# Optimization experiments

Hardware: AMD Instinct MI355X
Metric: run time of the kernel (lower is better)

Reference implementation:

```python
import jax, jax.numpy as jnp
import numpy as np

N_CELL = 50000
N_GENE = 50000
E = 800000
D = 256
EPS = 1e-5


def setup_inputs() -> dict:
    key = jax.random.key(0)
    ks = jax.random.split(key, 12)
    inp = {
        "x_cell": jax.random.normal(ks[0], (N_CELL, D), jnp.float32),
        "x_gene": jax.random.normal(ks[1], (N_GENE, D), jnp.float32),
        "W_cg": jax.random.normal(ks[2], (D, D), jnp.float32) * (1.0 / np.sqrt(D)),
        "W_gc": jax.random.normal(ks[3], (D, D), jnp.float32) * (1.0 / np.sqrt(D)),
        "W_gg": jax.random.normal(ks[4], (D, D), jnp.float32) * (1.0 / np.sqrt(D)),
        "gamma_cell": jnp.ones((D,), jnp.float32),
        "beta_cell": jnp.zeros((D,), jnp.float32),
        "gamma_gene": jnp.ones((D,), jnp.float32),
        "beta_gene": jnp.zeros((D,), jnp.float32),
        "b_cell": jnp.zeros((D,), jnp.float32),
        "b_gene": jnp.zeros((D,), jnp.float32),
        "src_cg": jax.random.randint(ks[5], (E,), 0, N_CELL, jnp.int64 if jax.config.jax_enable_x64 else jnp.int32),
        "dst_cg": jax.random.randint(ks[6], (E,), 0, N_GENE, jnp.int64 if jax.config.jax_enable_x64 else jnp.int32),
        "src_gc": jax.random.randint(ks[7], (E,), 0, N_GENE, jnp.int64 if jax.config.jax_enable_x64 else jnp.int32),
        "dst_gc": jax.random.randint(ks[8], (E,), 0, N_CELL, jnp.int64 if jax.config.jax_enable_x64 else jnp.int32),
        "src_gg": jax.random.randint(ks[9], (E,), 0, N_GENE, jnp.int64 if jax.config.jax_enable_x64 else jnp.int32),
        "dst_gg": jax.random.randint(ks[10], (E,), 0, N_GENE, jnp.int64 if jax.config.jax_enable_x64 else jnp.int32),
    }
    return inp


def _graph_conv(x_src, src, dst, n_src, n_dst, W):
    """DGL GraphConv with norm='both': D_dst^{-1/2} A D_src^{-1/2} X W."""
    ones = jnp.ones(src.shape[0], x_src.dtype)
    deg_out = jnp.clip(jax.ops.segment_sum(ones, src, num_segments=n_src), 1.0)
    deg_in = jnp.clip(jax.ops.segment_sum(ones, dst, num_segments=n_dst), 1.0)
    h = x_src * jax.lax.rsqrt(deg_out)[:, None]          # [n_src, D]
    agg = jax.ops.segment_sum(h[src], dst, num_segments=n_dst)  # gather+scatter
    agg = agg * jax.lax.rsqrt(deg_in)[:, None]           # [n_dst, D]
    return agg @ W


def _post(h, gamma, beta, b):
    # LayerNorm (affine) -> + h_bias -> relu -> dropout(p=0, eval = identity)
    mu = jnp.mean(h, axis=-1, keepdims=True)
    var = jnp.mean((h - mu) ** 2, axis=-1, keepdims=True)
    h = (h - mu) * jax.lax.rsqrt(var + EPS) * gamma + beta
    return jax.nn.relu(h + b)


def reference(x_cell, x_gene, W_cg, W_gc, W_gg, gamma_cell, beta_cell,
              gamma_gene, beta_gene, b_cell, b_gene,
              src_cg, dst_cg, src_gc, dst_gc, src_gg, dst_gg):
    # HeteroGraphConv with aggregate='sum' across relations per dst ntype
    h_gene = (_graph_conv(x_cell, src_cg, dst_cg, N_CELL, N_GENE, W_cg)
              + _graph_conv(x_gene, src_gg, dst_gg, N_GENE, N_GENE, W_gg))
    h_cell = _graph_conv(x_gene, src_gc, dst_gc, N_GENE, N_CELL, W_gc)
    out_cell = _post(h_cell, gamma_cell, beta_cell, b_cell)
    out_gene = _post(h_gene, gamma_gene, beta_gene, b_gene)
    return jnp.stack([out_cell, out_gene])  # [2, 50000, 256]
```

## Files before the change

### kernel.cpp

```cpp
#include <hip/hip_runtime.h>
#include <hip/hip_bf16.h>
#include <stdint.h>

#define DDIM 256
#define NSHARD 8
#define T1 4096
#define NCPAD 128
#define CCAP 9216

typedef short s8v __attribute__((ext_vector_type(8)));
typedef float f4v __attribute__((ext_vector_type(4)));

__device__ __forceinline__ float bf2f(unsigned u) { return __uint_as_float(u << 16); }
__device__ __forceinline__ unsigned short f2bf(float f) {
    __hip_bfloat16 h = __float2bfloat16(f);
    return *reinterpret_cast<unsigned short*>(&h);
}
__device__ __forceinline__ unsigned pack2(float a, float b) {
    return (unsigned)f2bf(a) | ((unsigned)f2bf(b) << 16);
}

__global__ void transpose3_k(const float* __restrict__ W0, const float* __restrict__ W1,
                             const float* __restrict__ W2, __hip_bfloat16* __restrict__ T0,
                             __hip_bfloat16* __restrict__ T1v, __hip_bfloat16* __restrict__ T2) {
    const float* W = (blockIdx.y == 0) ? W0 : (blockIdx.y == 1) ? W1 : W2;
    __hip_bfloat16* T = (blockIdx.y == 0) ? T0 : (blockIdx.y == 1) ? T1v : T2;
    T[blockIdx.x * DDIM + threadIdx.x] = __float2bfloat16(W[threadIdx.x * DDIM + blockIdx.x]);
}

__global__ __launch_bounds__(256) void bin1_k(
    const int* __restrict__ s0, const int* __restrict__ d0,
    const int* __restrict__ s1, const int* __restrict__ d1,
    const int* __restrict__ s2, const int* __restrict__ d2,
    int* __restrict__ cs_shard,
    int* __restrict__ gcur,
    unsigned* __restrict__ recs,
    int N, int E) {
    __shared__ unsigned stage[T1];
    __shared__ int hcnt[NCPAD], hoff[NCPAD], lbase[NCPAD], lcur[NCPAD];
    const int t = threadIdx.x;
    const int rel = blockIdx.y;
    const int* s = (rel == 0) ? s0 : (rel == 1) ? s1 : s2;
    const int* d = (rel == 0) ? d0 : (rel == 1) ? d1 : d2;
    const int e0 = blockIdx.x * T1;
    const int n = min(T1, E - e0);
    int* csb = cs_shard + ((size_t)(blockIdx.x & (NSHARD - 1)) * 3 + rel) * N;

    if (t < NCPAD) { hcnt[t] = 0; lcur[t] = 0; }
    __syncthreads();

    int ssr[T1 / 256], ddr[T1 / 256];
    #pragma unroll
    for (int k = 0; k < T1 / 256; ++k) {
        const int li = k * 256 + t;
        const bool v = li < n;
        ssr[k] = v ? s[e0 + li] : -1;
        ddr[k] = v ? d[e0 + li] : -1;
        if (v) {
            atomicAdd(&hcnt[ddr[k] >> 9], 1);
            atomicAdd(&csb[ssr[k]], 1);
        }
    }
    __syncthreads();

    if (t < 64) {
        const int a0 = hcnt[2 * t], a1 = hcnt[2 * t + 1];
        const int sum = a0 + a1;
        int incl = sum;
        #pragma unroll
        for (int off = 1; off < 64; off <<= 1) {
            const int u = __shfl_up(incl, off);
            if (t >= off) incl += u;
        }
        const int excl = incl - sum;
        hoff[2 * t] = excl;
        hoff[2 * t + 1] = excl + a0;
    }
    __syncthreads();
    if (t < NCPAD) lbase[t] = atomicAdd(&gcur[rel * NCPAD + t], hcnt[t]);
    __syncthreads();

    #pragma unroll
    for (int k = 0; k < T1 / 256; ++k) {
        if (ddr[k] >= 0) {
            const int b = ddr[k] >> 9;
            const int p = atomicAdd(&lcur[b], 1);
            stage[hoff[b] + p] = (unsigned)ssr[k] | ((unsigned)(ddr[k] & 511) << 16)
                                 | ((unsigned)b << 25);
        }
    }
    __syncthreads();

    for (int i = t; i < n; i += 256) {
        const unsigned r = stage[i];
        const int b = (int)(r >> 25);
        const int pos = lbase[b] + (i - hoff[b]);
        if (pos < CCAP)
            recs[((size_t)rel * NCPAD + b) * CCAP + pos] = r & 0x1FFFFFFu;
    }
}

__global__ void reduce_cs_k(const int* __restrict__ cs_shard, int* __restrict__ cs, int n3) {
    const int i = blockIdx.x * blockDim.x + threadIdx.x;
    if (i >= n3) return;
    int v = 0;
    #pragma unroll
    for (int s = 0; s < NSHARD; ++s) v += cs_shard[(size_t)s * n3 + i];
    cs[i] = v;
}

__global__ __launch_bounds__(256) void sort_k(
    unsigned* __restrict__ recs, const int* __restrict__ gcur,
    int* __restrict__ row_beg, int* __restrict__ row_cnt, int N, int ncb) {
    __shared__ unsigned stage[CCAP];
    __shared__ int rc[512], ro[512], rcur[512];
    const int t = threadIdx.x;
    const int rel = blockIdx.x / ncb, bin = blockIdx.x % ncb;
    const size_t base = ((size_t)rel * NCPAD + bin) * CCAP;
    const int n = min(gcur[rel * NCPAD + bin], CCAP);

    for (int i = t; i < 512; i += 256) rc[i] = 0;
    __syncthreads();
    for (int i = t; i < n; i += 256) {
        const unsigned r = recs[base + i];
        stage[i] = r;
        atomicAdd(&rc[(r >> 16) & 511], 1);
    }
    __syncthreads();
    if (t < 64) {
        int v[8], p[8], sum = 0;
        #pragma unroll
        for (int j = 0; j < 8; ++j) { v[j] = rc[t * 8 + j]; p[j] = sum; sum += v[j]; }
        int incl = sum;
        #pragma unroll
        for (int off = 1; off < 64; off <<= 1) {
            const int u = __shfl_up(incl, off);
            if (t >= off) incl += u;
        }
        const int excl = incl - sum;
        #pragma unroll
        for (int j = 0; j < 8; ++j) { ro[t * 8 + j] = excl + p[j]; rcur[t * 8 + j] = excl + p[j]; }
    }
    __syncthreads();
    for (int i = t; i < 512; i += 256) {
        const int grow = bin * 512 + i;
        if (grow < N) {
            row_cnt[(size_t)rel * N + grow] = rc[i];
            row_beg[(size_t)rel * N + grow] = (int)(base + ro[i]);
        }
    }
    for (int i = t; i < n; i += 256) {
        const unsigned r = stage[i];
        const int pos = atomicAdd(&rcur[(r >> 16) & 511], 1);
        recs[base + pos] = r & 0xffffu;
    }
}

__global__ __launch_bounds__(256, 4) void gemm2_k(
    const float* __restrict__ X,
    const __hip_bfloat16* __restrict__ Wt0, const __hip_bfloat16* __restrict__ Wt1,
    const int* __restrict__ deg0, const int* __restrict__ deg1,
    __hip_bfloat16* __restrict__ Y0, __hip_bfloat16* __restrict__ Y1, int M) {
    __shared__ __hip_bfloat16 wlds[2][2][16][DDIM];
    const int t = threadIdx.x;
    const int lane = t & 63, wid = t >> 6;
    const int c = lane & 15, kb = lane >> 4;
    const int rA = blockIdx.x * 128 + wid * 32 + c;
    const int rB = rA + 16;
    const bool vA = rA < M, vB = rB < M;
    const int rAc = vA ? rA : (M - 1), rBc = vB ? rB : (M - 1);

    s8v xfA[8], xfB[8];
    const float* xA = X + (size_t)rAc * DDIM;
    const float* xB = X + (size_t)rBc * DDIM;
    #pragma unroll
    for (int ks = 0; ks < 8; ++ks) {
        const int k0 = ks * 32 + kb * 8;
        const f4v a0 = *reinterpret_cast<const f4v*>(xA + k0);
        const f4v a1 = *reinterpret_cast<const f4v*>(xA + k0 + 4);
        const f4v b0 = *reinterpret_cast<const f4v*>(xB + k0);
        const f4v b1 = *reinterpret_cast<const f4v*>(xB + k0 + 4);
        union { s8v v; unsigned short u[8]; } fa, fb;
        #pragma unroll
        for (int j = 0; j < 4; ++j) {
            fa.u[j] = f2bf(a0[j]); fa.u[4 + j] = f2bf(a1[j]);
            fb.u[j] = f2bf(b0[j]); fb.u[4 + j] = f2bf(b1[j]);
        }
        xfA[ks] = fa.v; xfB[ks] = fb.v;
    }

    const int dA0 = deg0[rAc], dB0 = deg0[rBc], dA1 = deg1[rAc], dB1 = deg1[rBc];
    const float s0A = rsqrtf((float)(dA0 < 1 ? 1 : dA0));
    const float s0B = rsqrtf((float)(dB0 < 1 ? 1 : dB0));
    const float s1A = rsqrtf((float)(dA1 < 1 ? 1 : dA1));
    const float s1B = rsqrtf((float)(dB1 < 1 ? 1 : dB1));

    {
        #pragma unroll
        for (int j = 0; j < 4; ++j) {
            const int q = t + j * 256;
            const int rel = q >> 9, rt = (q >> 5) & 15, ch = q & 31;
            const __hip_bfloat16* Wsrc = rel ? Wt1 : Wt0;
            const uint4 v = *reinterpret_cast<const uint4*>(Wsrc + (size_t)rt * DDIM + ch * 8);
            *reinterpret_cast<uint4*>(&wlds[0][rel][rt][(ch ^ (rt & 7)) * 8]) = v;
        }
    }

    #pragma unroll 2
    for (int nt = 0; nt < 16; ++nt) {
        __syncthreads();
        uint4 sv[4];
        if (nt + 1 < 16) {
            #pragma unroll
            for (int j = 0; j < 4; ++j) {
                const int q = t + j * 256;
                const int rel = q >> 9, rt = (q >> 5) & 15, ch = q & 31;
                const __hip_bfloat16* Wsrc = rel ? Wt1 : Wt0;
                sv[j] = *reinterpret_cast<const uint4*>(
                    Wsrc + (size_t)((nt + 1) * 16 + rt) * DDIM + ch * 8);
            }
        }

        const int buf = nt & 1;
        f4v a00 = (f4v){0.f,0.f,0.f,0.f}, a01 = a00, a10 = a00, a11 = a00;
        #pragma unroll
        for (int ks = 0; ks < 8; ++ks) {
            const int chs = ((kb + 4 * ks) ^ (c & 7)) * 8;
            const s8v wf0 = *reinterpret_cast<const s8v*>(&wlds[buf][0][c][chs]);
            const s8v wf1 = *reinterpret_cast<const s8v*>(&wlds[buf][1][c][chs]);
            a00 = __builtin_amdgcn_mfma_f32_16x16x32_bf16(wf0, xfA[ks], a00, 0, 0, 0);
            a10 = __builtin_amdgcn_mfma_f32_16x16x32_bf16(wf0, xfB[ks], a10, 0, 0, 0);
            a01 = __builtin_amdgcn_mfma_f32_16x16x32_bf16(wf1, xfA[ks], a01, 0, 0, 0);
            a11 = __builtin_amdgcn_mfma_f32_16x16x32_bf16(wf1, xfB[ks], a11, 0, 0, 0);
        }
        const int col = nt * 16 + kb * 4;
        if (vA) {
            uint2 o0, o1;
            o0.x = pack2(a00[0] * s0A, a00[1] * s0A); o0.y = pack2(a00[2] * s0A, a00[3] * s0A);
            o1.x = pack2(a01[0] * s1A, a01[1] * s1A); o1.y = pack2(a01[2] * s1A, a01[3] * s1A);
            *reinterpret_cast<uint2*>(Y0 + (size_t)rA * DDIM + col) = o0;
            *reinterpret_cast<uint2*>(Y1 + (size_t)rA * DDIM + col) = o1;
        }
        if (vB) {
            uint2 o0, o1;
            o0.x = pack2(a10[0] * s0B, a10[1] * s0B); o0.y = pack2(a10[2] * s0B, a10[3] * s0B);
            o1.x = pack2(a11[0] * s1B, a11[1] * s1B); o1.y = pack2(a11[2] * s1B, a11[3] * s1B);
            *reinterpret_cast<uint2*>(Y0 + (size_t)rB * DDIM + col) = o0;
            *reinterpret_cast<uint2*>(Y1 + (size_t)rB * DDIM + col) = o1;
        }

        if (nt + 1 < 16) {
            #pragma unroll
            for (int j = 0; j < 4; ++j) {
                const int q = t + j * 256;
                const int rel = q >> 9, rt = (q >> 5) & 15, ch = q & 31;
                *reinterpret_cast<uint4*>(&wlds[buf ^ 1][rel][rt][(ch ^ (rt & 7)) * 8]) = sv[j];
            }
        }
    }
}

__global__ __launch_bounds__(256, 4) void gemm1_k(
    const float* __restrict__ X, const __hip_bfloat16* __restrict__ Wt0,
    const int* __restrict__ deg0, __hip_bfloat16* __restrict__ Y0, int M) {
    __shared__ __hip_bfloat16 wlds[2][16][DDIM];
    const int t = threadIdx.x;
    const int lane = t & 63, wid = t >> 6;
    const int c = lane & 15, kb = lane >> 4;
    const int rA = blockIdx.x * 128 + wid * 32 + c;
    const int rB = rA + 16;
    const bool vA = rA < M, vB = rB < M;
    const int rAc = vA ? rA : (M - 1), rBc = vB ? rB : (M - 1);

    s8v xfA[8], xfB[8];
    const float* xA = X + (size_t)rAc * DDIM;
    const float* xB = X + (size_t)rBc * DDIM;
    #pragma unroll
    for (int ks = 0; ks < 8; ++ks) {
        const int k0 = ks * 32 + kb * 8;
        const f4v a0 = *reinterpret_cast<const f4v*>(xA + k0);
        const f4v a1 = *reinterpret_cast<const f4v*>(xA + k0 + 4);
        const f4v b0 = *reinterpret_cast<const f4v*>(xB + k0);
        const f4v b1 = *reinterpret_cast<const f4v*>(xB + k0 + 4);
        union { s8v v; unsigned short u[8]; } fa, fb;
        #pragma unroll
        for (int j = 0; j < 4; ++j) {
            fa.u[j] = f2bf(a0[j]); fa.u[4 + j] = f2bf(a1[j]);
            fb.u[j] = f2bf(b0[j]); fb.u[4 + j] = f2bf(b1[j]);
        }
        xfA[ks] = fa.v; xfB[ks] = fb.v;
    }
    const int dA0 = deg0[rAc], dB0 = deg0[rBc];
    const float s0A = rsqrtf((float)(dA0 < 1 ? 1 : dA0));
    const float s0B = rsqrtf((float)(dB0 < 1 ? 1 : dB0));

    {
        #pragma unroll
        for (int j = 0; j < 2; ++j) {
            const int q = t + j * 256;
            const int rt = (q >> 5) & 15, ch = q & 31;
            const uint4 v = *reinterpret_cast<const uint4*>(Wt0 + (size_t)rt * DDIM + ch * 8);
            *reinterpret_cast<uint4*>(&wlds[0][rt][(ch ^ (rt & 7)) * 8]) = v;
        }
    }

    #pragma unroll 2
    for (int nt = 0; nt < 16; ++nt) {
        __syncthreads();
        uint4 sv[2];
        if (nt + 1 < 16) {
            #pragma unroll
            for (int j = 0; j < 2; ++j) {
                const int q = t + j * 256;
                const int rt = (q >> 5) & 15, ch = q & 31;
                sv[j] = *reinterpret_cast<const uint4*>(
                    Wt0 + (size_t)((nt + 1) * 16 + rt) * DDIM + ch * 8);
            }
        }

        const int buf = nt & 1;
        f4v a00 = (f4v){0.f,0.f,0.f,0.f}, a10 = a00;
        #pragma unroll
        for (int ks = 0; ks < 8; ++ks) {
            const int chs = ((kb + 4 * ks) ^ (c & 7)) * 8;
            const s8v wf0 = *reinterpret_cast<const s8v*>(&wlds[buf][c][chs]);
            a00 = __builtin_amdgcn_mfma_f32_16x16x32_bf16(wf0, xfA[ks], a00, 0, 0, 0);
            a10 = __builtin_amdgcn_mfma_f32_16x16x32_bf16(wf0, xfB[ks], a10, 0, 0, 0);
        }
        const int col = nt * 16 + kb * 4;
        if (vA) {
            uint2 o;
            o.x = pack2(a00[0] * s0A, a00[1] * s0A); o.y = pack2(a00[2] * s0A, a00[3] * s0A);
            *reinterpret_cast<uint2*>(Y0 + (size_t)rA * DDIM + col) = o;
        }
        if (vB) {
            uint2 o;
            o.x = pack2(a10[0] * s0B, a10[1] * s0B); o.y = pack2(a10[2] * s0B, a10[3] * s0B);
            *reinterpret_cast<uint2*>(Y0 + (size_t)rB * DDIM + col) = o;
        }

        if (nt + 1 < 16) {
            #pragma unroll
            for (int j = 0; j < 2; ++j) {
                const int q = t + j * 256;
                const int rt = (q >> 5) & 15, ch = q & 31;
                *reinterpret_cast<uint4*>(&wlds[buf ^ 1][rt][(ch ^ (rt & 7)) * 8]) = sv[j];
            }
        }
    }
}

__device__ __forceinline__ void addv(f4v& a, uint2 v) {
    a[0] += bf2f(v.x & 0xffffu);
    a[1] += bf2f(v.x >> 16);
    a[2] += bf2f(v.y & 0xffffu);
    a[3] += bf2f(v.y >> 16);
}

__device__ __forceinline__ f4v segsum(const unsigned* __restrict__ recs, int beg, int n,
                                      const __hip_bfloat16* __restrict__ Y, int lane) {
    f4v a = (f4v){0.f, 0.f, 0.f, 0.f};
    for (int j0 = 0; j0 < n; j0 += 64) {
        const int chunk = min(64, n - j0);
        unsigned rv = 0;
        if (lane < chunk) rv = recs[beg + j0 + lane];
        int t = 0;
        for (; t + 8 <= chunk; t += 8) {
            uint2 v[8];
            #pragma unroll
            for (int i = 0; i < 8; ++i) {
                const int s = (int)(__shfl(rv, t + i) & 0xffffu);
                v[i] = reinterpret_cast<const uint2*>(Y + (size_t)s * DDIM)[lane];
            }
            #pragma unroll
            for (int i = 0; i < 8; ++i) addv(a, v[i]);
        }
        if (t + 4 <= chunk) {
            uint2 v[4];
            #pragma unroll
            for (int i = 0; i < 4; ++i) {
                const int s = (int)(__shfl(rv, t + i) & 0xffffu);
                v[i] = reinterpret_cast<const uint2*>(Y + (size_t)s * DDIM)[lane];
            }
            #pragma unroll
            for (int i = 0; i < 4; ++i) addv(a, v[i]);
            t += 4;
        }
        for (; t < chunk; ++t) {
            const int s = (int)(__shfl(rv, t) & 0xffffu);
            addv(a, reinterpret_cast<const uint2*>(Y + (size_t)s * DDIM)[lane]);
        }
    }
    return a;
}

__global__ __launch_bounds__(256, 4) void gather_ln_k(
    const unsigned* __restrict__ recs,
    const int* __restrict__ beg0, const int* __restrict__ cnt0,
    const __hip_bfloat16* __restrict__ Y0,
    const int* __restrict__ beg1, const int* __restrict__ cnt1,
    const __hip_bfloat16* __restrict__ Y1,
    const float* __restrict__ gamma, const float* __restrict__ beta,
    const float* __restrict__ bias, float* __restrict__ out, int n_dst) {
    const int lane = threadIdx.x & 63, wid = threadIdx.x >> 6;
    const int row = blockIdx.x * 4 + wid;
    if (row >= n_dst) return;

    const int n0 = cnt0[row];
    f4v a = segsum(recs, beg0[row], n0, Y0, lane);
    a *= rsqrtf((float)(n0 < 1 ? 1 : n0));
    if (beg1 != nullptr) {
        const int n1 = cnt1[row];
        f4v a1 = segsum(recs, beg1[row], n1, Y1, lane);
        a += a1 * rsqrtf((float)(n1 < 1 ? 1 : n1));
    }

    float s1 = a[0] + a[1] + a[2] + a[3];
    float s2 = a[0]*a[0] + a[1]*a[1] + a[2]*a[2] + a[3]*a[3];
    #pragma unroll
    for (int off = 1; off < 64; off <<= 1) {
        s1 += __shfl_xor(s1, off);
        s2 += __shfl_xor(s2, off);
    }
    const float mu = s1 * (1.f / 256.f);
    float var = s2 * (1.f / 256.f) - mu * mu;
    var = fmaxf(var, 0.f);
    const float rs = rsqrtf(var + 1e-5f);

    const f4v g  = reinterpret_cast<const f4v*>(gamma)[lane];
    const f4v be = reinterpret_cast<const f4v*>(beta)[lane];
    const f4v bb = reinterpret_cast<const f4v*>(bias)[lane];
    f4v o;
    #pragma unroll
    for (int j = 0; j < 4; ++j) {
        float v = (a[j] - mu) * rs * g[j] + be[j] + bb[j];
        o[j] = fmaxf(v, 0.f);
    }
    reinterpret_cast<f4v*>(out + (size_t)row * DDIM)[lane] = o;
}

extern "C" void kernel_launch(void* const* d_in, const int* in_sizes, int n_in,
                              void* d_out, int out_size, void* d_ws, size_t ws_size,
                              hipStream_t stream) {
    const float* x_cell     = (const float*)d_in[0];
    const float* x_gene     = (const float*)d_in[1];
    const float* W_cg       = (const float*)d_in[2];
    const float* W_gc       = (const float*)d_in[3];
    const float* W_gg       = (const float*)d_in[4];
    const float* gamma_cell = (const float*)d_in[5];
    const float* beta_cell  = (const float*)d_in[6];
    const float* gamma_gene = (const float*)d_in[7];
    const float* beta_gene  = (const float*)d_in[8];
    const float* b_cell     = (const float*)d_in[9];
    const float* b_gene     = (const float*)d_in[10];
    const int* src_cg = (const int*)d_in[11];
    const int* dst_cg = (const int*)d_in[12];
    const int* src_gc = (const int*)d_in[13];
    const int* dst_gc = (const int*)d_in[14];
    const int* src_gg = (const int*)d_in[15];
    const int* dst_gg = (const int*)d_in[16];

    const int N = in_sizes[0] / DDIM;
    const int E = in_sizes[11];
    const int ncb = (N + 511) >> 9;

    char* wsb = (char*)d_ws;
    size_t off = 0;
    __hip_bfloat16* Y_gc = (__hip_bfloat16*)(wsb + off); off += (size_t)N * DDIM * 2;
    unsigned* recs = (unsigned*)(wsb + off);             off += (size_t)3 * NCPAD * CCAP * 4;
    int* row_beg = (int*)(wsb + off);                    off += (size_t)3 * N * 4;
    int* row_cnt = (int*)(wsb + off);                    off += (size_t)3 * N * 4;
    int* cs      = (int*)(wsb + off);                    off += (size_t)3 * N * 4;
    const size_t zeroOff = off;
    int* cs_shard = (int*)(wsb + off);                   off += (size_t)NSHARD * 3 * N * 4;
    int* gcur     = (int*)(wsb + off);                   off += (size_t)3 * NCPAD * 4;
    const size_t zeroBytes = off - zeroOff;
    __hip_bfloat16* Wt_gc = (__hip_bfloat16*)(wsb + off); off += (size_t)DDIM * DDIM * 2;
    __hip_bfloat16* Wt_cg = (__hip_bfloat16*)(wsb + off); off += (size_t)DDIM * DDIM * 2;
    __hip_bfloat16* Wt_gg = (__hip_bfloat16*)(wsb + off);

    int* cs_gc = cs, *cs_cg = cs + N, *cs_gg = cs + 2 * N;
    int* beg_gc = row_beg, *beg_cg = row_beg + N, *beg_gg = row_beg + 2 * N;
    int* cnt_gc = row_cnt, *cnt_cg = row_cnt + N, *cnt_gg = row_cnt + 2 * N;

    float* out_cell = (float*)d_out;
    float* out_gene = out_cell + (size_t)N * DDIM;
    __hip_bfloat16* Y_cg = (__hip_bfloat16*)d_out;
    __hip_bfloat16* Y_gg = Y_cg + (size_t)N * DDIM;

    const int binBlocks  = (E + T1 - 1) / T1;
    const int gemmBlocks = (N + 127) / 128;
    const int gatherBlocks = (N + 3) / 4;

    transpose3_k<<<dim3(DDIM, 3), DDIM, 0, stream>>>(W_gc, W_cg, W_gg, Wt_gc, Wt_cg, Wt_gg);
    hipMemsetAsync(wsb + zeroOff, 0, zeroBytes, stream);

    bin1_k<<<dim3(binBlocks, 3), 256, 0, stream>>>(src_gc, dst_gc, src_cg, dst_cg,
                                                   src_gg, dst_gg, cs_shard, gcur, recs, N, E);
    reduce_cs_k<<<(3 * N + 255) / 256, 256, 0, stream>>>(cs_shard, cs, 3 * N);
    sort_k<<<3 * ncb, 256, 0, stream>>>(recs, gcur, row_beg, row_cnt, N, ncb);

    gemm2_k<<<gemmBlocks, 256, 0, stream>>>(x_gene, Wt_gc, Wt_gg, cs_gc, cs_gg,
                                            Y_gc, Y_gg, N);
    gemm1_k<<<gemmBlocks, 256, 0, stream>>>(x_cell, Wt_cg, cs_cg, Y_cg, N);

    gather_ln_k<<<gatherBlocks, 256, 0, stream>>>(recs, beg_cg, cnt_cg, Y_cg,
                                                  beg_gg, cnt_gg, Y_gg,
                                                  gamma_gene, beta_gene, b_gene, out_gene, N);
    gather_ln_k<<<gatherBlocks, 256, 0, stream>>>(recs, beg_gc, cnt_gc, Y_gc,
                                                  nullptr, nullptr, nullptr,
                                                  gamma_cell, beta_cell, b_cell, out_cell, N);
}
```

Baseline: 404.9 us.

## Merge sort and both GEMMs into one launch; fold degree reduce; 16-bit edge records

Removes the separate reduce_cs kernel: the GEMMs now sum the eight per-shard degree counts directly. The sort, gemm2 and gemm1 stages are combined into a single mid_k launch whose block ranges dispatch to each body, so the independent work runs concurrently and two launches disappear. The sort writes 16-bit source indices into a separate buffer after staging them in LDS, which halves the index traffic in the gather kernels. In exchange the GEMMs do extra strided degree reads, the fused kernel shares one LDS size and launch bounds across all roles, and an extra recs16 buffer is used.

```diff
diff --git a/kernel.cpp b/kernel.cpp
--- a/kernel.cpp
+++ b/kernel.cpp
@@ -100,32 +100,33 @@
     }
 }
 
-__global__ void reduce_cs_k(const int* __restrict__ cs_shard, int* __restrict__ cs, int n3) {
-    const int i = blockIdx.x * blockDim.x + threadIdx.x;
-    if (i >= n3) return;
+__device__ __forceinline__ int deg_sum(const int* __restrict__ cs_shard, int rel, int r, int N) {
     int v = 0;
     #pragma unroll
-    for (int s = 0; s < NSHARD; ++s) v += cs_shard[(size_t)s * n3 + i];
-    cs[i] = v;
-}
-
-__global__ __launch_bounds__(256) void sort_k(
-    unsigned* __restrict__ recs, const int* __restrict__ gcur,
-    int* __restrict__ row_beg, int* __restrict__ row_cnt, int N, int ncb) {
-    __shared__ unsigned stage[CCAP];
-    __shared__ int rc[512], ro[512], rcur[512];
+    for (int s = 0; s < NSHARD; ++s) v += cs_shard[((size_t)s * 3 + rel) * N + r];
+    return v;
+}
+
+
+__device__ void sort_body(int sb, unsigned char* smem,
+                          const unsigned* __restrict__ recs32,
+                          unsigned short* __restrict__ recs16,
+                          const int* __restrict__ gcur,
+                          int* __restrict__ row_beg, int* __restrict__ row_cnt,
+                          int N, int ncb) {
+    unsigned short* stage = (unsigned short*)smem;
+    int* rc   = (int*)(smem + 18432);
+    int* ro   = (int*)(smem + 20480);
+    int* rcur = (int*)(smem + 22528);
     const int t = threadIdx.x;
-    const int rel = blockIdx.x / ncb, bin = blockIdx.x % ncb;
+    const int rel = sb / ncb, bin = sb % ncb;
     const size_t base = ((size_t)rel * NCPAD + bin) * CCAP;
     const int n = min(gcur[rel * NCPAD + bin], CCAP);
 
     for (int i = t; i < 512; i += 256) rc[i] = 0;
     __syncthreads();
-    for (int i = t; i < n; i += 256) {
-        const unsigned r = recs[base + i];
-        stage[i] = r;
-        atomicAdd(&rc[(r >> 16) & 511], 1);
-    }
+    for (int i = t; i < n; i += 256)
+        atomicAdd(&rc[(recs32[base + i] >> 16) & 511], 1);
     __syncthreads();
     if (t < 64) {
         int v[8], p[8], sum = 0;
@@ -150,22 +151,27 @@
         }
     }
     for (int i = t; i < n; i += 256) {
-        const unsigned r = stage[i];
+        const unsigned r = recs32[base + i];
         const int pos = atomicAdd(&rcur[(r >> 16) & 511], 1);
-        recs[base + pos] = r & 0xffffu;
-    }
-}
-
-__global__ __launch_bounds__(256, 4) void gemm2_k(
-    const float* __restrict__ X,
-    const __hip_bfloat16* __restrict__ Wt0, const __hip_bfloat16* __restrict__ Wt1,
-    const int* __restrict__ deg0, const int* __restrict__ deg1,
-    __hip_bfloat16* __restrict__ Y0, __hip_bfloat16* __restrict__ Y1, int M) {
-    __shared__ __hip_bfloat16 wlds[2][2][16][DDIM];
+        stage[pos] = (unsigned short)(r & 0xffffu);
+    }
+    __syncthreads();
+    for (int i = t; i < n; i += 256)
+        recs16[base + i] = stage[i];
+}
+
+__device__ void gemm2_body(int gb, unsigned char* smem, const float* __restrict__ X,
+                           const __hip_bfloat16* __restrict__ Wt0,
+                           const __hip_bfloat16* __restrict__ Wt1,
+                           const int* __restrict__ cs_shard, int rel0, int rel1,
+                           __hip_bfloat16* __restrict__ Y0, __hip_bfloat16* __restrict__ Y1,
+                           int M, int N) {
+    typedef __hip_bfloat16 (*lds_t)[2][16][DDIM];
+    lds_t wlds = (lds_t)smem;
     const int t = threadIdx.x;
     const int lane = t & 63, wid = t >> 6;
     const int c = lane & 15, kb = lane >> 4;
-    const int rA = blockIdx.x * 128 + wid * 32 + c;
+    const int rA = gb * 128 + wid * 32 + c;
     const int rB = rA + 16;
     const bool vA = rA < M, vB = rB < M;
     const int rAc = vA ? rA : (M - 1), rBc = vB ? rB : (M - 1);
@@ -189,7 +195,8 @@
         xfA[ks] = fa.v; xfB[ks] = fb.v;
     }
 
-    const int dA0 = deg0[rAc], dB0 = deg0[rBc], dA1 = deg1[rAc], dB1 = deg1[rBc];
+    const int dA0 = deg_sum(cs_shard, rel0, rAc, N), dB0 = deg_sum(cs_shard, rel0, rBc, N);
+    const int dA1 = deg_sum(cs_shard, rel1, rAc, N), dB1 = deg_sum(cs_shard, rel1, rBc, N);
     const float s0A = rsqrtf((float)(dA0 < 1 ? 1 : dA0));
     const float s0B = rsqrtf((float)(dB0 < 1 ? 1 : dB0));
     const float s1A = rsqrtf((float)(dA1 < 1 ? 1 : dA1));
@@ -202,7 +209,7 @@
             const int rel = q >> 9, rt = (q >> 5) & 15, ch = q & 31;
             const __hip_bfloat16* Wsrc = rel ? Wt1 : Wt0;
             const uint4 v = *reinterpret_cast<const uint4*>(Wsrc + (size_t)rt * DDIM + ch * 8);
-            *reinterpret_cast<uint4*>(&wlds[0][rel][rt][(ch ^ (rt & 7)) * 8]) = v;
+            *reinterpret_cast<uint4*>(&(*wlds)[0 * 2 + rel][rt][(ch ^ (rt & 7)) * 8]) = v;
         }
     }
 
@@ -226,8 +233,8 @@
         #pragma unroll
         for (int ks = 0; ks < 8; ++ks) {
             const int chs = ((kb + 4 * ks) ^ (c & 7)) * 8;
-            const s8v wf0 = *reinterpret_cast<const s8v*>(&wlds[buf][0][c][chs]);
-            const s8v wf1 = *reinterpret_cast<const s8v*>(&wlds[buf][1][c][chs]);
+            const s8v wf0 = *reinterpret_cast<const s8v*>(&(*wlds)[buf * 2 + 0][c][chs]);
+            const s8v wf1 = *reinterpret_cast<const s8v*>(&(*wlds)[buf * 2 + 1][c][chs]);
             a00 = __builtin_amdgcn_mfma_f32_16x16x32_bf16(wf0, xfA[ks], a00, 0, 0, 0);
             a10 = __builtin_amdgcn_mfma_f32_16x16x32_bf16(wf0, xfB[ks], a10, 0, 0, 0);
             a01 = __builtin_amdgcn_mfma_f32_16x16x32_bf16(wf1, xfA[ks], a01, 0, 0, 0);
@@ -254,20 +261,22 @@
             for (int j = 0; j < 4; ++j) {
                 const int q = t + j * 256;
                 const int rel = q >> 9, rt = (q >> 5) & 15, ch = q & 31;
-                *reinterpret_cast<uint4*>(&wlds[buf ^ 1][rel][rt][(ch ^ (rt & 7)) * 8]) = sv[j];
+                *reinterpret_cast<uint4*>(&(*wlds)[(buf ^ 1) * 2 + rel][rt][(ch ^ (rt & 7)) * 8]) = sv[j];
             }
         }
     }
 }
 
-__global__ __launch_bounds__(256, 4) void gemm1_k(
-    const float* __restrict__ X, const __hip_bfloat16* __restrict__ Wt0,
-    const int* __restrict__ deg0, __hip_bfloat16* __restrict__ Y0, int M) {
-    __shared__ __hip_bfloat16 wlds[2][16][DDIM];
+__device__ void gemm1_body(int gb, unsigned char* smem, const float* __restrict__ X,
+                           const __hip_bfloat16* __restrict__ Wt0,
+                           const int* __restrict__ cs_shard, int rel0,
+                           __hip_bfloat16* __restrict__ Y0, int M, int N) {
+    typedef __hip_bfloat16 (*lds_t)[16][DDIM];
+    lds_t wlds = (lds_t)smem;
     const int t = threadIdx.x;
     const int lane = t & 63, wid = t >> 6;
     const int c = lane & 15, kb = lane >> 4;
-    const int rA = blockIdx.x * 128 + wid * 32 + c;
+    const int rA = gb * 128 + wid * 32 + c;
     const int rB = rA + 16;
     const bool vA = rA < M, vB = rB < M;
     const int rAc = vA ? rA : (M - 1), rBc = vB ? rB : (M - 1);
@@ -290,7 +299,7 @@
         }
         xfA[ks] = fa.v; xfB[ks] = fb.v;
     }
-    const int dA0 = deg0[rAc], dB0 = deg0[rBc];
+    const int dA0 = deg_sum(cs_shard, rel0, rAc, N), dB0 = deg_sum(cs_shard, rel0, rBc, N);
     const float s0A = rsqrtf((float)(dA0 < 1 ? 1 : dA0));
     const float s0B = rsqrtf((float)(dB0 < 1 ? 1 : dB0));
 
@@ -300,7 +309,7 @@
             const int q = t + j * 256;
             const int rt = (q >> 5) & 15, ch = q & 31;
             const uint4 v = *reinterpret_cast<const uint4*>(Wt0 + (size_t)rt * DDIM + ch * 8);
-            *reinterpret_cast<uint4*>(&wlds[0][rt][(ch ^ (rt & 7)) * 8]) = v;
+            *reinterpret_cast<uint4*>(&(*wlds)[0 * 16 + rt][(ch ^ (rt & 7)) * 8]) = v;
         }
     }
 
@@ -323,7 +332,7 @@
         #pragma unroll
         for (int ks = 0; ks < 8; ++ks) {
             const int chs = ((kb + 4 * ks) ^ (c & 7)) * 8;
-            const s8v wf0 = *reinterpret_cast<const s8v*>(&wlds[buf][c][chs]);
+            const s8v wf0 = *reinterpret_cast<const s8v*>(&(*wlds)[buf * 16 + c][chs]);
             a00 = __builtin_amdgcn_mfma_f32_16x16x32_bf16(wf0, xfA[ks], a00, 0, 0, 0);
             a10 = __builtin_amdgcn_mfma_f32_16x16x32_bf16(wf0, xfB[ks], a10, 0, 0, 0);
         }
@@ -344,9 +353,33 @@
             for (int j = 0; j < 2; ++j) {
                 const int q = t + j * 256;
                 const int rt = (q >> 5) & 15, ch = q & 31;
-                *reinterpret_cast<uint4*>(&wlds[buf ^ 1][rt][(ch ^ (rt & 7)) * 8]) = sv[j];
+                *reinterpret_cast<uint4*>(&(*wlds)[(buf ^ 1) * 16 + rt][(ch ^ (rt & 7)) * 8]) = sv[j];
             }
         }
+    }
+}
+
+__global__ __launch_bounds__(256, 4) void mid_k(
+    const unsigned* __restrict__ recs32, unsigned short* __restrict__ recs16,
+    const int* __restrict__ gcur,
+    int* __restrict__ row_beg, int* __restrict__ row_cnt,
+    const float* __restrict__ x_gene, const float* __restrict__ x_cell,
+    const __hip_bfloat16* __restrict__ Wt_gc, const __hip_bfloat16* __restrict__ Wt_gg,
+    const __hip_bfloat16* __restrict__ Wt_cg,
+    const int* __restrict__ cs_shard,
+    __hip_bfloat16* __restrict__ Y_gc, __hip_bfloat16* __restrict__ Y_gg,
+    __hip_bfloat16* __restrict__ Y_cg,
+    int N, int ncb, int gemmBlocks) {
+    __shared__ uint4 smem4[2048];
+    unsigned char* smem = (unsigned char*)smem4;
+    const int bid = blockIdx.x;
+    if (bid < gemmBlocks) {
+        gemm2_body(bid, smem, x_gene, Wt_gc, Wt_gg, cs_shard, 0, 2, Y_gc, Y_gg, N, N);
+    } else if (bid < 2 * gemmBlocks) {
+        gemm1_body(bid - gemmBlocks, smem, x_cell, Wt_cg, cs_shard, 1, Y_cg, N, N);
+    } else {
+        sort_body(bid - 2 * gemmBlocks, smem, recs32, recs16, gcur,
+                  row_beg, row_cnt, N, ncb);
     }
 }
 
@@ -357,7 +390,7 @@
     a[3] += bf2f(v.y >> 16);
 }
 
-__device__ __forceinline__ f4v segsum(const unsigned* __restrict__ recs, int beg, int n,
+__device__ __forceinline__ f4v segsum(const unsigned short* __restrict__ recs, int beg, int n,
                                       const __hip_bfloat16* __restrict__ Y, int lane) {
     f4v a = (f4v){0.f, 0.f, 0.f, 0.f};
     for (int j0 = 0; j0 < n; j0 += 64) {
@@ -369,7 +402,7 @@
             uint2 v[8];
             #pragma unroll
             for (int i = 0; i < 8; ++i) {
-                const int s = (int)(__shfl(rv, t + i) & 0xffffu);
+                const int s = (int)__shfl(rv, t + i);
                 v[i] = reinterpret_cast<const uint2*>(Y + (size_t)s * DDIM)[lane];
             }
             #pragma unroll
@@ -379,7 +412,7 @@
             uint2 v[4];
             #pragma unroll
             for (int i = 0; i < 4; ++i) {
-                const int s = (int)(__shfl(rv, t + i) & 0xffffu);
+                const int s = (int)__shfl(rv, t + i);
                 v[i] = reinterpret_cast<const uint2*>(Y + (size_t)s * DDIM)[lane];
             }
             #pragma unroll
@@ -387,7 +420,7 @@
             t += 4;
         }
         for (; t < chunk; ++t) {
-            const int s = (int)(__shfl(rv, t) & 0xffffu);
+            const int s = (int)__shfl(rv, t);
             addv(a, reinterpret_cast<const uint2*>(Y + (size_t)s * DDIM)[lane]);
         }
     }
@@ -395,7 +428,7 @@
 }
 
 __global__ __launch_bounds__(256, 4) void gather_ln_k(
-    const unsigned* __restrict__ recs,
+    const unsigned short* __restrict__ recs,
     const int* __restrict__ beg0, const int* __restrict__ cnt0,
     const __hip_bfloat16* __restrict__ Y0,
     const int* __restrict__ beg1, const int* __restrict__ cnt1,
@@ -467,10 +500,10 @@
     char* wsb = (char*)d_ws;
     size_t off = 0;
     __hip_bfloat16* Y_gc = (__hip_bfloat16*)(wsb + off); off += (size_t)N * DDIM * 2;
-    unsigned* recs = (unsigned*)(wsb + off);             off += (size_t)3 * NCPAD * CCAP * 4;
+    unsigned* recs32 = (unsigned*)(wsb + off);           off += (size_t)3 * NCPAD * CCAP * 4;
+    unsigned short* recs16 = (unsigned short*)(wsb + off); off += (size_t)3 * NCPAD * CCAP * 2;
     int* row_beg = (int*)(wsb + off);                    off += (size_t)3 * N * 4;
     int* row_cnt = (int*)(wsb + off);                    off += (size_t)3 * N * 4;
-    int* cs      = (int*)(wsb + off);                    off += (size_t)3 * N * 4;
     const size_t zeroOff = off;
     int* cs_shard = (int*)(wsb + off);                   off += (size_t)NSHARD * 3 * N * 4;
     int* gcur     = (int*)(wsb + off);                   off += (size_t)3 * NCPAD * 4;
@@ -479,7 +512,6 @@
     __hip_bfloat16* Wt_cg = (__hip_bfloat16*)(wsb + off); off += (size_t)DDIM * DDIM * 2;
     __hip_bfloat16* Wt_gg = (__hip_bfloat16*)(wsb + off);
 
-    int* cs_gc = cs, *cs_cg = cs + N, *cs_gg = cs + 2 * N;
     int* beg_gc = row_beg, *beg_cg = row_beg + N, *beg_gg = row_beg + 2 * N;
     int* cnt_gc = row_cnt, *cnt_cg = row_cnt + N, *cnt_gg = row_cnt + 2 * N;
 
@@ -496,18 +528,16 @@
     hipMemsetAsync(wsb + zeroOff, 0, zeroBytes, stream);
 
     bin1_k<<<dim3(binBlocks, 3), 256, 0, stream>>>(src_gc, dst_gc, src_cg, dst_cg,
-                                                   src_gg, dst_gg, cs_shard, gcur, recs, N, E);
-    reduce_cs_k<<<(3 * N + 255) / 256, 256, 0, stream>>>(cs_shard, cs, 3 * N);
-    sort_k<<<3 * ncb, 256, 0, stream>>>(recs, gcur, row_beg, row_cnt, N, ncb);
-
-    gemm2_k<<<gemmBlocks, 256, 0, stream>>>(x_gene, Wt_gc, Wt_gg, cs_gc, cs_gg,
-                                            Y_gc, Y_gg, N);
-    gemm1_k<<<gemmBlocks, 256, 0, stream>>>(x_cell, Wt_cg, cs_cg, Y_cg, N);
-
-    gather_ln_k<<<gatherBlocks, 256, 0, stream>>>(recs, beg_cg, cnt_cg, Y_cg,
+                                                   src_gg, dst_gg, cs_shard, gcur, recs32, N, E);
+
+    mid_k<<<2 * gemmBlocks + 3 * ncb, 256, 0, stream>>>(
+        recs32, recs16, gcur, row_beg, row_cnt, x_gene, x_cell,
+        Wt_gc, Wt_gg, Wt_cg, cs_shard, Y_gc, Y_gg, Y_cg, N, ncb, gemmBlocks);
+
+    gather_ln_k<<<gatherBlocks, 256, 0, stream>>>(recs16, beg_cg, cnt_cg, Y_cg,
                                                   beg_gg, cnt_gg, Y_gg,
                                                   gamma_gene, beta_gene, b_gene, out_gene, N);
-    gather_ln_k<<<gatherBlocks, 256, 0, stream>>>(recs, beg_gc, cnt_gc, Y_gc,
+    gather_ln_k<<<gatherBlocks, 256, 0, stream>>>(recs16, beg_gc, cnt_gc, Y_gc,
                                                   nullptr, nullptr, nullptr,
                                                   gamma_cell, beta_cell, b_cell, out_cell, N);
 }
```

Result: faster. 395.6 us (-2.3%).
